# Optimization experiments

Measured on AMD Instinct MI355X. Metric: run time of the kernel, lower is better.

## Reference

```python
import jax, jax.numpy as jnp
import numpy as np
from jax.scipy.stats import norm

N_NODES = 8192   # n_nodes; also fs (receivers = arange(fs) indexes Z)
E = 262144       # n_entries: timestamped interaction events in the batch
BS = 4096        # len(nodes)
N_SEND = 2048    # unique senders used in integral term
K = 8            # n_change_points passed to __init__ -> K+1 change points
TMAX = 100.0
PENALTY = 10.0


def setup_inputs() -> dict:
    key = jax.random.key(0)
    ks = jax.random.split(key, 8)
    Z = jax.random.normal(ks[0], (N_NODES, 2, K + 1), jnp.float32)
    beta = jax.random.normal(ks[1], (), jnp.float32)
    timestamps = jax.random.uniform(ks[2], (E,), jnp.float32, 0.0, TMAX)
    senders = jax.random.randint(ks[3], (E,), 0, N_NODES, jnp.int32)
    receivers = jax.random.randint(ks[4], (E,), 0, N_NODES, jnp.int32)
    nodes = jax.random.randint(ks[5], (BS,), 0, N_NODES, jnp.int32)
    senders_unique = jnp.sort(jax.random.permutation(ks[6], N_NODES)[:N_SEND]).astype(jnp.int32)
    change_points = (jnp.arange(K + 1, dtype=jnp.float32) / K) * (TMAX + 1e-4)
    return dict(Z=Z, beta=beta, timestamps=timestamps, senders=senders,
                receivers=receivers, nodes=nodes, senders_unique=senders_unique,
                change_points=change_points, fs=N_NODES)


def _rowdot(a, b):  # [n,2],[n,2] -> [n]
    return jnp.sum(a * b, axis=1)


def _negloglike(Z, beta, timestamps, change_points, senders, receivers, nodes,
                senders_unique, fs):
    seg = change_points[1] - change_points[0]
    # gaussian random-walk prior on trajectories of the batch nodes
    prior = PENALTY * (jnp.sum(Z[nodes, :, 0] ** 2)
                       + jnp.sum((Z[nodes, :, 1:] - Z[nodes, :, :-1]) ** 2))
    # time-bin gather + linear interpolation per event
    kappa = jnp.floor(timestamps / seg).astype(jnp.int32)
    d = timestamps / seg - kappa  # deltas in [0,1)
    od = 1.0 - d
    Zs_c = Z[senders, :, kappa]      # [E,2]
    Zs_n = Z[senders, :, kappa + 1]
    Zr_c = Z[receivers, :, kappa]
    Zr_n = Z[receivers, :, kappa + 1]
    flt = (od ** 2 * (2 * _rowdot(Zs_c, Zr_c) - _rowdot(Zs_c, Zs_c) - _rowdot(Zr_c, Zr_c))
           + 2 * d * od * (_rowdot(Zs_c, Zr_n) + _rowdot(Zs_n, Zr_c)
                           - _rowdot(Zs_c, Zs_n) - _rowdot(Zr_c, Zr_n))
           + d ** 2 * (2 * _rowdot(Zs_n, Zr_n) - _rowdot(Zs_n, Zs_n) - _rowdot(Zr_n, Zr_n)))
    # integral term: scan over change points (keeps one [S,fs] tile set live)
    Zu = jnp.moveaxis(Z[senders_unique], 2, 0)  # [K+1, S, 2]
    Zr = jnp.moveaxis(Z[:fs], 2, 0)             # [K+1, fs, 2]
    dts = change_points[1:] - change_points[:-1]
    xs = (Zu[:-1], Zu[1:], Zr[:-1], Zr[1:], dts)

    def step(acc, x):
        Zs0, Zs1, Zr0, Zr1, dt = x
        D = (_rowdot(Zs0, Zs0)[:, None] + _rowdot(Zr0, Zr0)[None, :]
             - 2 * Zs0 @ Zr0.T)
        DZs = Zs1 - Zs0
        DZr = Zr1 - Zr0
        S = (_rowdot(DZs, DZs)[:, None] + _rowdot(DZr, DZr)[None, :]
             - 2 * DZs @ DZr.T)
        C = (DZs @ Zr0.T + Zs0 @ DZr.T
             - _rowdot(DZs, Zs0)[:, None] - _rowdot(DZr, Zr0)[None, :])
        mask = (D > 0.0) & (S > 0.0)  # replaces boolean filtering in torch
        Ss = jnp.where(mask, S, 1.0)  # safe denominator; masked out below
        mu = C / Ss
        sigma = jnp.sqrt(0.5 / Ss)
        val = (jnp.exp(Ss * mu ** 2 - D) * sigma
               * (norm.cdf((1.0 - mu) / sigma) - norm.cdf(-mu / sigma)) * dt)
        return acc + 0.5 * jnp.sum(jnp.where(mask, val, 0.0)), None

    integral, _ = jax.lax.scan(step, jnp.float32(0.0), xs)
    n_entries = jnp.float32(timestamps.shape[0])
    sqrt_2pi = jnp.sqrt(jnp.float32(2.0 * np.pi))
    scale = fs / nodes.shape[0]  # fs / bs
    return scale * (prior - beta * n_entries - jnp.sum(flt)
                    + sqrt_2pi * jnp.exp(beta) * integral)


def reference(Z, beta, timestamps, senders, receivers, nodes, senders_unique,
              change_points, fs):
    return _negloglike(Z, beta, timestamps, change_points, senders, receivers,
                       nodes, senders_unique, fs)
```

## Files before the change

### kernel.cpp

```cpp
#include <hip/hip_runtime.h>

#define EDGES   262144
#define CTPB    256
#define SCHUNK  256
#define NINT    2048
#define NFLT    (EDGES / CTPB)
#define NPRI    16
#define NBLK    (NINT + NFLT + NPRI)

typedef float v2f __attribute__((ext_vector_type(2)));

__device__ __forceinline__ float fast_rsq(float x) { return __builtin_amdgcn_rsqf(x); }

__device__ __forceinline__ v2f erf_poly2(v2f x) {
    v2f c;
    c.x = __builtin_amdgcn_fmed3f(x.x, -2.0f, 2.0f);
    c.y = __builtin_amdgcn_fmed3f(x.y, -2.0f, 2.0f);
    v2f t = c * c;
    v2f p = t * 0.0011996f - 0.0165450f;
    p = p * t + 0.100174f;
    p = p * t - 0.370237f;
    p = p * t + 1.127915f;
    return c * p;
}

template <int NW>
__device__ __forceinline__ float block_reduce(float v, float* sm) {
    #pragma unroll
    for (int o = 32; o > 0; o >>= 1) v += __shfl_down(v, o, 64);
    int lane = threadIdx.x & 63;
    int wid  = threadIdx.x >> 6;
    if (lane == 0) sm[wid] = v;
    __syncthreads();
    float r = 0.0f;
    if (threadIdx.x == 0) {
        #pragma unroll
        for (int w = 0; w < NW; ++w) r += sm[w];
    }
    return r;
}

__global__ __launch_bounds__(CTPB) void k_mega(const float* __restrict__ Z,
        const float* __restrict__ ts, const int* __restrict__ snd,
        const int* __restrict__ rcv, const int* __restrict__ nodes,
        const int* __restrict__ su, const float* __restrict__ cp,
        float* __restrict__ part, int mode) {
    __shared__ __align__(16) float sZx[SCHUNK];
    __shared__ __align__(16) float sZy[SCHUNK];
    __shared__ __align__(16) float sDx[SCHUNK];
    __shared__ __align__(16) float sDy[SCHUNK];
    __shared__ float smr[CTPB / 64];
    const int bid = blockIdx.x;
    const int tid = threadIdx.x;
    float r;
    int slot;

    if (bid < NINT) {
        const int k  = bid >> 8;
        const int sc = (bid >> 5) & 7;
        const int rb = bid & 31;
        {
            int n = su[sc * SCHUNK + tid];
            const float* z = Z + n * 18 + k;
            float zx = z[0], zy = z[9];
            sZx[tid] = zx; sZy[tid] = zy;
            sDx[tid] = z[1] - zx; sDy[tid] = z[10] - zy;
        }
        const float* zr = Z + (rb * CTPB + tid) * 18 + k;
        float rzx = zr[0], rzy = zr[9];
        float rdx = zr[1] - rzx, rdy = zr[10] - rzy;
        __syncthreads();

        const v2f* pZx = (const v2f*)sZx;
        const v2f* pZy = (const v2f*)sZy;
        const v2f* pDx = (const v2f*)sDx;
        const v2f* pDy = (const v2f*)sDy;
        float s0 = 0.0f, s1 = 0.0f;
        #pragma unroll 4
        for (int i = 0; i < SCHUNK / 2; ++i) {
            v2f wx = pZx[i] - rzx;
            v2f wy = pZy[i] - rzy;
            v2f vx = pDx[i] - rdx;
            v2f vy = pDy[i] - rdy;
            v2f D  = wx * wx + wy * wy;
            v2f S  = vx * vx + vy * vy;
            v2f mc = vx * wx + vy * wy;
            v2f rsq;
            rsq.x = fast_rsq(S.x);
            rsq.y = fast_rsq(S.y);
            v2f u  = -mc * rsq;
            v2f rt = S * rsq;
            v2f ea = u * u - D;
            v2f ex;
            ex.x = __expf(ea.x);
            ex.y = __expf(ea.y);
            v2f e = erf_poly2(rt - u) + erf_poly2(u);
            v2f q = ex * rsq * e;
            s0 += (D.x > 0.0f && S.x > 0.0f) ? q.x : 0.0f;
            s1 += (D.y > 0.0f && S.y > 0.0f) ? q.y : 0.0f;
        }
        r = block_reduce<CTPB / 64>(s0 + s1, smr);
        slot = 2;
    } else if (bid < NINT + NFLT) {
        int e = (bid - NINT) * CTPB + tid;
        float seg = cp[1] - cp[0];
        float x   = ts[e] / seg;
        float kf  = floorf(x);
        int kappa = (int)kf;
        float d   = x - kf;
        float od  = 1.0f - d;
        int sb = snd[e] * 18, rbse = rcv[e] * 18;
        float ux = Z[sb + kappa]     - Z[rbse + kappa];
        float uy = Z[sb + 9 + kappa] - Z[rbse + 9 + kappa];
        float vx = Z[sb + kappa + 1]     - Z[rbse + kappa + 1];
        float vy = Z[sb + 9 + kappa + 1] - Z[rbse + 9 + kappa + 1];
        float wx = od * ux + d * vx;
        float wy = od * uy + d * vy;
        r = block_reduce<CTPB / 64>(-fmaf(wx, wx, wy * wy), smr);
        slot = 1;
    } else {
        int i = (bid - NINT - NFLT) * CTPB + tid;
        int n = nodes[i];
        const float* z = Z + n * 18;
        float s = 0.0f;
        #pragma unroll
        for (int d = 0; d < 2; ++d) {
            float prev = z[d * 9];
            s = fmaf(prev, prev, s);
            #pragma unroll
            for (int k = 1; k <= 8; ++k) {
                float cur = z[d * 9 + k];
                float df  = cur - prev;
                s = fmaf(df, df, s);
                prev = cur;
            }
        }
        r = block_reduce<CTPB / 64>(s, smr);
        slot = 0;
    }
    if (tid == 0) {
        if (mode) part[bid] = r;
        else      atomicAdd(part + slot, r);
    }
}

__global__ __launch_bounds__(CTPB) void k_final(const float* __restrict__ ws,
        int mode, const float* __restrict__ betap, const int* __restrict__ fsp,
        const float* __restrict__ cp, float* __restrict__ out,
        float n_entries, float bs) {
    __shared__ float sm0[CTPB / 64], sm1[CTPB / 64], sm2[CTPB / 64];
    int tid = threadIdx.x;
    float pr, fl, qq;
    if (mode) {
        float q = 0.0f, f = 0.0f, p = 0.0f;
        for (int i = tid; i < NBLK; i += CTPB) {
            float v = ws[i];
            if (i < NINT)             q += v;
            else if (i < NINT + NFLT) f += v;
            else                      p += v;
        }
        qq = block_reduce<CTPB / 64>(q, sm0);
        fl = block_reduce<CTPB / 64>(f, sm1);
        pr = block_reduce<CTPB / 64>(p, sm2);
    } else {
        pr = ws[0]; fl = ws[1]; qq = ws[2];
    }
    if (tid == 0) {
        float prior  = 10.0f * pr;
        float beta   = betap[0];
        float fs     = (float)fsp[0];
        float seg    = cp[1] - cp[0];
        float integral = 0.17677669529663687f * seg * qq;
        const float sqrt2pi = 2.5066282746310002f;
        float res = prior - beta * n_entries - fl + sqrt2pi * expf(beta) * integral;
        out[0] = (fs / bs) * res;
    }
}

extern "C" void kernel_launch(void* const* d_in, const int* in_sizes, int n_in,
                              void* d_out, int out_size, void* d_ws, size_t ws_size,
                              hipStream_t stream) {
    const float* Z    = (const float*)d_in[0];
    const float* beta = (const float*)d_in[1];
    const float* ts   = (const float*)d_in[2];
    const int*   snd  = (const int*)d_in[3];
    const int*   rcv  = (const int*)d_in[4];
    const int*   nodes= (const int*)d_in[5];
    const int*   su   = (const int*)d_in[6];
    const float* cp   = (const float*)d_in[7];
    const int*   fs   = (const int*)d_in[8];
    float* acc = (float*)d_ws;

    const int mode = (ws_size >= NBLK * sizeof(float)) ? 1 : 0;
    if (!mode) hipMemsetAsync(acc, 0, 3 * sizeof(float), stream);
    k_mega<<<NBLK, CTPB, 0, stream>>>(Z, ts, snd, rcv, nodes, su, cp, acc, mode);
    k_final<<<1, CTPB, 0, stream>>>(acc, mode, beta, fs, cp, (float*)d_out,
                                    (float)in_sizes[2], (float)in_sizes[5]);
}
```

Baseline: 165.9 us.

## Fold flt and prior work into integral blocks and rescale the pair math

```diff
diff --git a/kernel.cpp b/kernel.cpp
--- a/kernel.cpp
+++ b/kernel.cpp
@@ -4,23 +4,26 @@
 #define CTPB    256
 #define SCHUNK  256
 #define NINT    2048
-#define NFLT    (EDGES / CTPB)
-#define NPRI    16
-#define NBLK    (NINT + NFLT + NPRI)
-
-typedef float v2f __attribute__((ext_vector_type(2)));
+#define EPB     (EDGES / NINT)
+#define NODESB  4096
+#define PPB     (NODESB / NINT)
+
+typedef float v4f __attribute__((ext_vector_type(4)));
+
+#define SS 1.2011224087864498f
 
 __device__ __forceinline__ float fast_rsq(float x) { return __builtin_amdgcn_rsqf(x); }
-
-__device__ __forceinline__ v2f erf_poly2(v2f x) {
-    v2f c;
-    c.x = __builtin_amdgcn_fmed3f(x.x, -2.0f, 2.0f);
-    c.y = __builtin_amdgcn_fmed3f(x.y, -2.0f, 2.0f);
-    v2f t = c * c;
-    v2f p = t * 0.0011996f - 0.0165450f;
-    p = p * t + 0.100174f;
-    p = p * t - 0.370237f;
-    p = p * t + 1.127915f;
+__device__ __forceinline__ float fast_ex2(float x) {
+    float r; asm("v_exp_f32 %0, %1" : "=v"(r) : "v"(x)); return r;
+}
+
+__device__ __forceinline__ float erf_s(float y) {
+    float c = __builtin_amdgcn_fmed3f(y, -2.4022448f, 2.4022448f);
+    float t = c * c;
+    float p = fmaf(t, 2.30540e-4f, -4.58723e-3f);
+    p = fmaf(p, t, 0.0400696f);
+    p = fmaf(p, t, -0.2136547f);
+    p = fmaf(p, t, 0.9390508f);
     return c * p;
 }
 
@@ -44,136 +47,137 @@
         const float* __restrict__ ts, const int* __restrict__ snd,
         const int* __restrict__ rcv, const int* __restrict__ nodes,
         const int* __restrict__ su, const float* __restrict__ cp,
-        float* __restrict__ part, int mode) {
-    __shared__ __align__(16) float sZx[SCHUNK];
-    __shared__ __align__(16) float sZy[SCHUNK];
-    __shared__ __align__(16) float sDx[SCHUNK];
-    __shared__ __align__(16) float sDy[SCHUNK];
+        const float* __restrict__ betap, float* __restrict__ part, int mode) {
+    __shared__ __align__(16) v4f sA[SCHUNK / 2];
+    __shared__ __align__(16) v4f sB[SCHUNK / 2];
     __shared__ float smr[CTPB / 64];
     const int bid = blockIdx.x;
     const int tid = threadIdx.x;
-    float r;
-    int slot;
-
-    if (bid < NINT) {
-        const int k  = bid >> 8;
-        const int sc = (bid >> 5) & 7;
-        const int rb = bid & 31;
-        {
-            int n = su[sc * SCHUNK + tid];
-            const float* z = Z + n * 18 + k;
-            float zx = z[0], zy = z[9];
-            sZx[tid] = zx; sZy[tid] = zy;
-            sDx[tid] = z[1] - zx; sDy[tid] = z[10] - zy;
-        }
-        const float* zr = Z + (rb * CTPB + tid) * 18 + k;
-        float rzx = zr[0], rzy = zr[9];
-        float rdx = zr[1] - rzx, rdy = zr[10] - rzy;
-        __syncthreads();
-
-        const v2f* pZx = (const v2f*)sZx;
-        const v2f* pZy = (const v2f*)sZy;
-        const v2f* pDx = (const v2f*)sDx;
-        const v2f* pDy = (const v2f*)sDy;
-        float s0 = 0.0f, s1 = 0.0f;
-        #pragma unroll 4
-        for (int i = 0; i < SCHUNK / 2; ++i) {
-            v2f wx = pZx[i] - rzx;
-            v2f wy = pZy[i] - rzy;
-            v2f vx = pDx[i] - rdx;
-            v2f vy = pDy[i] - rdy;
-            v2f D  = wx * wx + wy * wy;
-            v2f S  = vx * vx + vy * vy;
-            v2f mc = vx * wx + vy * wy;
-            v2f rsq;
-            rsq.x = fast_rsq(S.x);
-            rsq.y = fast_rsq(S.y);
-            v2f u  = -mc * rsq;
-            v2f rt = S * rsq;
-            v2f ea = u * u - D;
-            v2f ex;
-            ex.x = __expf(ea.x);
-            ex.y = __expf(ea.y);
-            v2f e = erf_poly2(rt - u) + erf_poly2(u);
-            v2f q = ex * rsq * e;
-            s0 += (D.x > 0.0f && S.x > 0.0f) ? q.x : 0.0f;
-            s1 += (D.y > 0.0f && S.y > 0.0f) ? q.y : 0.0f;
-        }
-        r = block_reduce<CTPB / 64>(s0 + s1, smr);
-        slot = 2;
-    } else if (bid < NINT + NFLT) {
-        int e = (bid - NINT) * CTPB + tid;
-        float seg = cp[1] - cp[0];
-        float x   = ts[e] / seg;
-        float kf  = floorf(x);
-        int kappa = (int)kf;
-        float d   = x - kf;
-        float od  = 1.0f - d;
-        int sb = snd[e] * 18, rbse = rcv[e] * 18;
-        float ux = Z[sb + kappa]     - Z[rbse + kappa];
-        float uy = Z[sb + 9 + kappa] - Z[rbse + 9 + kappa];
-        float vx = Z[sb + kappa + 1]     - Z[rbse + kappa + 1];
-        float vy = Z[sb + 9 + kappa + 1] - Z[rbse + 9 + kappa + 1];
-        float wx = od * ux + d * vx;
-        float wy = od * uy + d * vy;
-        r = block_reduce<CTPB / 64>(-fmaf(wx, wx, wy * wy), smr);
-        slot = 1;
-    } else {
-        int i = (bid - NINT - NFLT) * CTPB + tid;
-        int n = nodes[i];
-        const float* z = Z + n * 18;
+    const int k  = bid >> 8;
+    const int sc = (bid >> 5) & 7;
+    const int rb = bid & 31;
+
+    float e_ts = 0.0f; int e_s = 0, e_r = 0, p_n = 0;
+    if (tid < EPB) {
+        int e = bid * EPB + tid;
+        e_ts = ts[e]; e_s = snd[e]; e_r = rcv[e];
+    } else if (tid < EPB + PPB) {
+        p_n = nodes[bid * PPB + (tid - EPB)];
+    }
+
+    {
+        int n = su[sc * SCHUNK + tid];
+        const float* z = Z + n * 18 + k;
+        float zx = z[0] * SS, zy = z[9] * SS;
+        float dx = z[1] * SS - zx, dy = z[10] * SS - zy;
+        float* fA = (float*)sA; float* fB = (float*)sB;
+        int p = tid >> 1, q = tid & 1;
+        fA[p * 4 + q] = zx; fA[p * 4 + 2 + q] = zy;
+        fB[p * 4 + q] = dx; fB[p * 4 + 2 + q] = dy;
+    }
+    const float* zr = Z + (rb * CTPB + tid) * 18 + k;
+    float rzx = zr[0] * SS, rzy = zr[9] * SS;
+    float rdx = zr[1] * SS - rzx, rdy = zr[10] * SS - rzy;
+
+    const float seg = cp[1] - cp[0];
+
+    float extra = 0.0f;
+    if (tid < EPB) {
+        float x  = e_ts / seg;
+        float kf = floorf(x);
+        int kap  = (int)kf;
+        float d  = x - kf, od = 1.0f - d;
+        const float* zs = Z + e_s * 18 + kap;
+        const float* zq = Z + e_r * 18 + kap;
+        float ux = zs[0] - zq[0],  uy = zs[9]  - zq[9];
+        float vx = zs[1] - zq[1],  vy = zs[10] - zq[10];
+        float wx = fmaf(od, ux, d * vx);
+        float wy = fmaf(od, uy, d * vy);
+        extra = fmaf(wx, wx, wy * wy);
+    } else if (tid < EPB + PPB) {
+        const float* z = Z + p_n * 18;
         float s = 0.0f;
         #pragma unroll
-        for (int d = 0; d < 2; ++d) {
-            float prev = z[d * 9];
+        for (int dd = 0; dd < 2; ++dd) {
+            float prev = z[dd * 9];
             s = fmaf(prev, prev, s);
             #pragma unroll
-            for (int k = 1; k <= 8; ++k) {
-                float cur = z[d * 9 + k];
+            for (int kk = 1; kk <= 8; ++kk) {
+                float cur = z[dd * 9 + kk];
                 float df  = cur - prev;
                 s = fmaf(df, df, s);
                 prev = cur;
             }
         }
-        r = block_reduce<CTPB / 64>(s, smr);
-        slot = 0;
-    }
+        extra = 10.0f * s;
+    }
+
+    __syncthreads();
+
+    const float Kc = 0.53223360f * seg * __expf(betap[0]);
+
+    const v4f* pA = (const v4f*)sA;
+    const v4f* pB = (const v4f*)sB;
+    float s0 = 0.0f, s1 = 0.0f;
+    #pragma unroll 4
+    for (int i = 0; i < SCHUNK / 2; ++i) {
+        v4f A = pA[i];
+        v4f B = pB[i];
+        {
+            float wx = A.x - rzx, wy = A.z - rzy;
+            float vx = B.x - rdx, vy = B.z - rdy;
+            float D  = fmaf(wy, wy, wx * wx);
+            float S  = fmaf(vy, vy, vx * vx);
+            float mc = fmaf(vy, wy, vx * wx);
+            float rs = fast_rsq(S);
+            float m  = mc * rs;
+            float rt = S * rs;
+            float ea = fmaf(m, m, -D);
+            float ex = fast_ex2(ea);
+            float e  = erf_s(rt + m) - erf_s(m);
+            float q  = ex * rs * e;
+            s0 += (S > 0.0f) ? q : 0.0f;
+        }
+        {
+            float wx = A.y - rzx, wy = A.w - rzy;
+            float vx = B.y - rdx, vy = B.w - rdy;
+            float D  = fmaf(wy, wy, wx * wx);
+            float S  = fmaf(vy, vy, vx * vx);
+            float mc = fmaf(vy, wy, vx * wx);
+            float rs = fast_rsq(S);
+            float m  = mc * rs;
+            float rt = S * rs;
+            float ea = fmaf(m, m, -D);
+            float ex = fast_ex2(ea);
+            float e  = erf_s(rt + m) - erf_s(m);
+            float q  = ex * rs * e;
+            s1 += (S > 0.0f) ? q : 0.0f;
+        }
+    }
+
+    float v = fmaf(Kc, s0 + s1, extra);
+    float r = block_reduce<CTPB / 64>(v, smr);
     if (tid == 0) {
         if (mode) part[bid] = r;
-        else      atomicAdd(part + slot, r);
+        else      atomicAdd(part, r);
     }
 }
 
 __global__ __launch_bounds__(CTPB) void k_final(const float* __restrict__ ws,
         int mode, const float* __restrict__ betap, const int* __restrict__ fsp,
-        const float* __restrict__ cp, float* __restrict__ out,
-        float n_entries, float bs) {
-    __shared__ float sm0[CTPB / 64], sm1[CTPB / 64], sm2[CTPB / 64];
+        float* __restrict__ out, float n_entries, float bs) {
+    __shared__ float sm[CTPB / 64];
     int tid = threadIdx.x;
-    float pr, fl, qq;
+    float a = 0.0f;
     if (mode) {
-        float q = 0.0f, f = 0.0f, p = 0.0f;
-        for (int i = tid; i < NBLK; i += CTPB) {
-            float v = ws[i];
-            if (i < NINT)             q += v;
-            else if (i < NINT + NFLT) f += v;
-            else                      p += v;
-        }
-        qq = block_reduce<CTPB / 64>(q, sm0);
-        fl = block_reduce<CTPB / 64>(f, sm1);
-        pr = block_reduce<CTPB / 64>(p, sm2);
-    } else {
-        pr = ws[0]; fl = ws[1]; qq = ws[2];
+        for (int i = tid; i < NINT; i += CTPB) a += ws[i];
+        a = block_reduce<CTPB / 64>(a, sm);
+    } else if (tid == 0) {
+        a = ws[0];
     }
     if (tid == 0) {
-        float prior  = 10.0f * pr;
-        float beta   = betap[0];
-        float fs     = (float)fsp[0];
-        float seg    = cp[1] - cp[0];
-        float integral = 0.17677669529663687f * seg * qq;
-        const float sqrt2pi = 2.5066282746310002f;
-        float res = prior - beta * n_entries - fl + sqrt2pi * expf(beta) * integral;
-        out[0] = (fs / bs) * res;
+        float res = a - betap[0] * n_entries;
+        out[0] = ((float)fsp[0] / bs) * res;
     }
 }
 
@@ -191,9 +195,10 @@
     const int*   fs   = (const int*)d_in[8];
     float* acc = (float*)d_ws;
 
-    const int mode = (ws_size >= NBLK * sizeof(float)) ? 1 : 0;
-    if (!mode) hipMemsetAsync(acc, 0, 3 * sizeof(float), stream);
-    k_mega<<<NBLK, CTPB, 0, stream>>>(Z, ts, snd, rcv, nodes, su, cp, acc, mode);
-    k_final<<<1, CTPB, 0, stream>>>(acc, mode, beta, fs, cp, (float*)d_out,
+    const int mode = (ws_size >= NINT * sizeof(float)) ? 1 : 0;
+    if (!mode) hipMemsetAsync(acc, 0, sizeof(float), stream);
+    k_mega<<<NINT, CTPB, 0, stream>>>(Z, ts, snd, rcv, nodes, su, cp, beta,
+                                      acc, mode);
+    k_final<<<1, CTPB, 0, stream>>>(acc, mode, beta, fs, (float*)d_out,
                                     (float)in_sizes[2], (float)in_sizes[5]);
 }
```

Result: slower. 175.7 us (+5.9%).
